# Kernel tuning notes

Measured on AMD Instinct MI355X. Metric: run time of the kernel, lower is better.

Reference implementation:

```python
import jax, jax.numpy as jnp
import numpy as np

N = 50000
E = 600000
D = 128


def setup_inputs() -> dict:
    key = jax.random.key(0)
    ks = jax.random.split(key, 10)
    scale = 1.0 / np.sqrt(D)
    inp = {
        "x": jax.random.normal(ks[0], (N, D), dtype=jnp.float32),
        "edge_index": jax.random.randint(ks[1], (2, E), 0, N, dtype=jnp.int64),
        # layer 0: fc + res_fc (residual=True, activation=relu)
        "W1": jax.random.normal(ks[2], (D, D), dtype=jnp.float32) * scale,
        "R1": jax.random.normal(ks[3], (D, D), dtype=jnp.float32) * scale,
        # layer 1
        "W2": jax.random.normal(ks[4], (D, D), dtype=jnp.float32) * scale,
        "R2": jax.random.normal(ks[5], (D, D), dtype=jnp.float32) * scale,
        # layer 2 (last, encoding=False -> no residual/activation)
        "W3": jax.random.normal(ks[6], (D, D), dtype=jnp.float32) * scale,
        # head Linear(out_dim, out_dim) with bias
        "Wh": jax.random.normal(ks[7], (D, D), dtype=jnp.float32) * scale,
        "bh": jnp.zeros((D,), dtype=jnp.float32),
    }
    return inp


def _gcn_stack(x, row, col, norm, W1, R1, W2, R2, W3, Wh, bh):
    n = x.shape[0]

    def conv(x, W, R, act):
        h = x @ W                                   # [N, D]
        msg = h[row] * norm[:, None]                # gather + per-edge scale [E+N, D]
        agg = jax.ops.segment_sum(msg, col, num_segments=n)  # scatter-add [N, D]
        if R is not None:
            agg = agg + x @ R                       # residual
        if act:
            agg = jax.nn.relu(agg)
        return agg

    x = conv(x, W1, R1, True)
    x = conv(x, W2, R2, True)
    x = conv(x, W3, None, False)
    return x @ Wh + bh


def reference(x, edge_index, W1, R1, W2, R2, W3, Wh, bh):
    n = x.shape[0]
    # add self loops (same edge structure for every layer)
    loops = jnp.arange(n, dtype=edge_index.dtype)
    row = jnp.concatenate([edge_index[0], loops])
    col = jnp.concatenate([edge_index[1], loops])
    # symmetric degree normalization: deg computed over col (incl. self loops)
    deg = jax.ops.segment_sum(jnp.ones_like(col, dtype=x.dtype), col, num_segments=n)
    dinv = deg ** -0.5
    norm = dinv[row] * dinv[col]                    # [E+N]
    return _gcn_stack(x, row, col, norm, W1, R1, W2, R2, W3, Wh, bh)
```

## Files before the change

### kernel.cpp

```cpp
#include <hip/hip_runtime.h>
#include <hip/hip_bf16.h>


#define SCAN_CHUNK 1024

typedef _Float16 half8 __attribute__((ext_vector_type(8)));
typedef _Float16 half4 __attribute__((ext_vector_type(4)));
typedef _Float16 half2v __attribute__((ext_vector_type(2)));
typedef float floatx4 __attribute__((ext_vector_type(4)));

__global__ void zero_int_kernel(int* __restrict__ p, int n) {
    int i = blockIdx.x * blockDim.x + threadIdx.x;
    if (i < n) p[i] = 0;
}

__global__ void hist_kernel(const int* __restrict__ col, int* __restrict__ cnt, int E) {
    int i = blockIdx.x * blockDim.x + threadIdx.x;
    if (i < E) atomicAdd(&cnt[col[i]], 1);
}

__global__ void dinv_kernel(const int* __restrict__ cnt, float* __restrict__ dinv, int n) {
    int i = blockIdx.x * blockDim.x + threadIdx.x;
    if (i < n) dinv[i] = rsqrtf((float)(cnt[i] + 1));
}

__global__ __launch_bounds__(256) void scan_reduce_kernel(
        const int* __restrict__ cnt, int* __restrict__ bsum, int n) {
    __shared__ int s[256];
    int b = blockIdx.x, t = threadIdx.x;
    int base = b * SCAN_CHUNK + t * 4;
    int v = 0;
    if (base + 3 < n) {
        int4 q = *(const int4*)&cnt[base];
        v = q.x + q.y + q.z + q.w;
    } else {
        for (int i = 0; i < 4; ++i) if (base + i < n) v += cnt[base + i];
    }
    s[t] = v;
    __syncthreads();
    for (int off = 128; off > 0; off >>= 1) {
        if (t < off) s[t] += s[t + off];
        __syncthreads();
    }
    if (t == 0) bsum[b] = s[0];
}

__global__ __launch_bounds__(1024) void scan_bsum_kernel(
        const int* __restrict__ bsum, int* __restrict__ boff, int nb) {
    __shared__ int s[1024];
    int t = threadIdx.x;
    s[t] = (t < nb) ? bsum[t] : 0;
    __syncthreads();
    for (int off = 1; off < 1024; off <<= 1) {
        int add = (t >= off) ? s[t - off] : 0;
        __syncthreads();
        s[t] += add;
        __syncthreads();
    }
    if (t < nb) boff[t] = (t == 0) ? 0 : s[t - 1];
}

__global__ __launch_bounds__(256) void scan_write_kernel(
        const int* __restrict__ cnt, const int* __restrict__ boff,
        int* __restrict__ row_ptr, int* __restrict__ cursor, int n, int E) {
    __shared__ int s[256];
    int b = blockIdx.x, t = threadIdx.x;
    int base = b * SCAN_CHUNK + t * 4;
    int v[4];
    int sum = 0;
    for (int i = 0; i < 4; ++i) {
        v[i] = (base + i < n) ? cnt[base + i] : 0;
        sum += v[i];
    }
    s[t] = sum;
    __syncthreads();
    for (int off = 1; off < 256; off <<= 1) {
        int add = (t >= off) ? s[t - off] : 0;
        __syncthreads();
        s[t] += add;
        __syncthreads();
    }
    int prefix = boff[b] + ((t == 0) ? 0 : s[t - 1]);
    for (int i = 0; i < 4; ++i) {
        if (base + i < n) {
            row_ptr[base + i] = prefix;
            cursor[base + i] = prefix;
            prefix += v[i];
        }
    }
    if (b == 0 && t == 0) row_ptr[n] = E;
}

__global__ void fill_kernel(const int* __restrict__ row, const int* __restrict__ colv,
                            const float* __restrict__ dinv, int* __restrict__ cursor,
                            int2* __restrict__ csr, int E) {
    int i = blockIdx.x * blockDim.x + threadIdx.x;
    if (i < E) {
        int r = row[i], c = colv[i];
        int p = atomicAdd(&cursor[c], 1);
        float nrm = dinv[r] * dinv[c];
        csr[p] = make_int2(r, __float_as_int(nrm));
    }
}

__global__ __launch_bounds__(256) void wcvt_kernel(
        const float* __restrict__ W1, const float* __restrict__ R1,
        const float* __restrict__ W2, const float* __restrict__ R2,
        const float* __restrict__ W3, const float* __restrict__ Wh,
        _Float16* __restrict__ Wt) {
    __shared__ float tile[32][33];
    int b = blockIdx.x;
    int mat = b >> 4, tl = b & 15;
    const float* W = (mat == 0) ? W1 : (mat == 1) ? R1 : (mat == 2) ? W2
                   : (mat == 3) ? R2 : (mat == 4) ? W3 : Wh;
    _Float16* T = Wt + (size_t)mat * 16384;
    int tr = (tl >> 2) * 32, tc = (tl & 3) * 32;
    int t = threadIdx.x;
    int i = t >> 3, j4 = t & 7;
    float4 v = *(const float4*)&W[(tr + i) * 128 + tc + j4 * 4];
    tile[i][j4 * 4 + 0] = v.x;
    tile[i][j4 * 4 + 1] = v.y;
    tile[i][j4 * 4 + 2] = v.z;
    tile[i][j4 * 4 + 3] = v.w;
    __syncthreads();
    half4 h;
    h.x = (_Float16)tile[j4 * 4 + 0][i];
    h.y = (_Float16)tile[j4 * 4 + 1][i];
    h.z = (_Float16)tile[j4 * 4 + 2][i];
    h.w = (_Float16)tile[j4 * 4 + 3][i];
    *(half4*)&T[(tc + i) * 128 + tr + j4 * 4] = h;
}

__global__ void cvt_kernel(const float* __restrict__ x, _Float16* __restrict__ xh, int n) {
    int i = (blockIdx.x * blockDim.x + threadIdx.x) * 4;
    if (i + 3 < n) {
        float4 v = *(const float4*)&x[i];
        half4 h;
        h.x = (_Float16)v.x; h.y = (_Float16)v.y;
        h.z = (_Float16)v.z; h.w = (_Float16)v.w;
        *(half4*)&xh[i] = h;
    } else {
        for (int j = i; j < n; ++j) xh[j] = (_Float16)x[j];
    }
}

__global__ __launch_bounds__(256) void gemm_h_kernel(
        const _Float16* __restrict__ X, const _Float16* __restrict__ Wt,
        _Float16* __restrict__ out, int n) {
    __shared__ _Float16 Af[64 * 136];
    __shared__ _Float16 Bt[128 * 136];
    int t = threadIdx.x;
    int r0 = blockIdx.x * 64;

#pragma unroll
    for (int i = 0; i < 4; ++i) {
        int flat = i * 256 + t;
        int r = flat >> 4, k8 = flat & 15;
        half8 v = {0, 0, 0, 0, 0, 0, 0, 0};
        if (r0 + r < n) v = *(const half8*)&X[(size_t)(r0 + r) * 128 + k8 * 8];
        *(half8*)&Af[r * 136 + k8 * 8] = v;
    }
#pragma unroll
    for (int i = 0; i < 8; ++i) {
        int flat = i * 256 + t;
        int c = flat >> 4, k8 = flat & 15;
        *(half8*)&Bt[c * 136 + k8 * 8] = *(const half8*)&Wt[c * 128 + k8 * 8];
    }
    __syncthreads();

    int lane = t & 63, w = t >> 6;
    int m = lane & 15, q = lane >> 4;

    floatx4 acc[8];
#pragma unroll
    for (int nt = 0; nt < 8; ++nt) acc[nt] = (floatx4){0.f, 0.f, 0.f, 0.f};

#pragma unroll
    for (int s = 0; s < 4; ++s) {
        half8 a = *(const half8*)&Af[(w * 16 + m) * 136 + s * 32 + q * 8];
#pragma unroll
        for (int nt = 0; nt < 8; ++nt) {
            half8 b = *(const half8*)&Bt[(nt * 16 + m) * 136 + s * 32 + q * 8];
            acc[nt] = __builtin_amdgcn_mfma_f32_16x16x32_f16(a, b, acc[nt], 0, 0, 0);
        }
    }

    int rowb = r0 + w * 16 + q * 4;
#pragma unroll
    for (int nt = 0; nt < 8; ++nt) {
        int col = nt * 16 + m;
#pragma unroll
        for (int r = 0; r < 4; ++r) {
            int gr = rowb + r;
            if (gr < n) out[(size_t)gr * 128 + col] = (_Float16)acc[nt][r];
        }
    }
}

__global__ __launch_bounds__(256) void gemm_f_kernel(
        const _Float16* __restrict__ X, const _Float16* __restrict__ Wt,
        const float* __restrict__ bias, float* __restrict__ out, int n) {
    __shared__ _Float16 Af[64 * 136];
    __shared__ _Float16 Bt[128 * 136];
    int t = threadIdx.x;
    int r0 = blockIdx.x * 64;

#pragma unroll
    for (int i = 0; i < 4; ++i) {
        int flat = i * 256 + t;
        int r = flat >> 4, k8 = flat & 15;
        half8 v = {0, 0, 0, 0, 0, 0, 0, 0};
        if (r0 + r < n) v = *(const half8*)&X[(size_t)(r0 + r) * 128 + k8 * 8];
        *(half8*)&Af[r * 136 + k8 * 8] = v;
    }
#pragma unroll
    for (int i = 0; i < 8; ++i) {
        int flat = i * 256 + t;
        int c = flat >> 4, k8 = flat & 15;
        *(half8*)&Bt[c * 136 + k8 * 8] = *(const half8*)&Wt[c * 128 + k8 * 8];
    }
    __syncthreads();

    int lane = t & 63, w = t >> 6;
    int m = lane & 15, q = lane >> 4;

    floatx4 acc[8];
#pragma unroll
    for (int nt = 0; nt < 8; ++nt) acc[nt] = (floatx4){0.f, 0.f, 0.f, 0.f};

#pragma unroll
    for (int s = 0; s < 4; ++s) {
        half8 a = *(const half8*)&Af[(w * 16 + m) * 136 + s * 32 + q * 8];
#pragma unroll
        for (int nt = 0; nt < 8; ++nt) {
            half8 b = *(const half8*)&Bt[(nt * 16 + m) * 136 + s * 32 + q * 8];
            acc[nt] = __builtin_amdgcn_mfma_f32_16x16x32_f16(a, b, acc[nt], 0, 0, 0);
        }
    }

    int rowb = r0 + w * 16 + q * 4;
#pragma unroll
    for (int nt = 0; nt < 8; ++nt) {
        int col = nt * 16 + m;
        float bb = bias[col];
#pragma unroll
        for (int r = 0; r < 4; ++r) {
            int gr = rowb + r;
            if (gr < n) out[(size_t)gr * 128 + col] = acc[nt][r] + bb;
        }
    }
}

__global__ void spmm_kernel(const _Float16* __restrict__ h, const _Float16* __restrict__ xr,
                            const int* __restrict__ row_ptr, const int2* __restrict__ csr,
                            const float* __restrict__ dinv, _Float16* __restrict__ out,
                            int n, int do_relu) {
    int gid = blockIdx.x * blockDim.x + threadIdx.x;
    int node = gid >> 6;
    int lane = gid & 63;
    if (node >= n) return;
    const half2v* hp = (const half2v*)h;
    float di = dinv[node];
    float w = di * di;
    half2v hv = hp[(size_t)node * 64 + lane];
    float accx = (float)hv.x * w, accy = (float)hv.y * w;
    int e = row_ptr[node], eend = row_ptr[node + 1];
    for (; e + 4 <= eend; e += 4) {
        int2 d0 = csr[e], d1 = csr[e + 1], d2 = csr[e + 2], d3 = csr[e + 3];
        half2v v0 = hp[(size_t)d0.x * 64 + lane];
        half2v v1 = hp[(size_t)d1.x * 64 + lane];
        half2v v2 = hp[(size_t)d2.x * 64 + lane];
        half2v v3 = hp[(size_t)d3.x * 64 + lane];
        float n0 = __int_as_float(d0.y), n1 = __int_as_float(d1.y);
        float n2 = __int_as_float(d2.y), n3 = __int_as_float(d3.y);
        accx = fmaf(n0, (float)v0.x, accx); accy = fmaf(n0, (float)v0.y, accy);
        accx = fmaf(n1, (float)v1.x, accx); accy = fmaf(n1, (float)v1.y, accy);
        accx = fmaf(n2, (float)v2.x, accx); accy = fmaf(n2, (float)v2.y, accy);
        accx = fmaf(n3, (float)v3.x, accx); accy = fmaf(n3, (float)v3.y, accy);
    }
    for (; e < eend; ++e) {
        int2 ed = csr[e];
        float nrm = __int_as_float(ed.y);
        half2v v = hp[(size_t)ed.x * 64 + lane];
        accx = fmaf(nrm, (float)v.x, accx);
        accy = fmaf(nrm, (float)v.y, accy);
    }
    if (xr) {
        half2v r = ((const half2v*)xr)[(size_t)node * 64 + lane];
        accx += (float)r.x;
        accy += (float)r.y;
    }
    if (do_relu) {
        accx = fmaxf(accx, 0.f);
        accy = fmaxf(accy, 0.f);
    }
    half2v o;
    o.x = (_Float16)accx;
    o.y = (_Float16)accy;
    ((half2v*)out)[(size_t)node * 64 + lane] = o;
}

extern "C" void kernel_launch(void* const* d_in, const int* in_sizes, int n_in,
                              void* d_out, int out_size, void* d_ws, size_t ws_size,
                              hipStream_t stream) {
    const float* x  = (const float*)d_in[0];
    const int*   ei = (const int*)d_in[1];
    const float* W1 = (const float*)d_in[2];
    const float* R1 = (const float*)d_in[3];
    const float* W2 = (const float*)d_in[4];
    const float* R2 = (const float*)d_in[5];
    const float* W3 = (const float*)d_in[6];
    const float* Wh = (const float*)d_in[7];
    const float* bh = (const float*)d_in[8];
    float* out = (float*)d_out;

    int N = in_sizes[0] / 128;
    int E = in_sizes[1] / 2;

    char* p = (char*)d_ws;
    auto alloc = [&](size_t bytes) {
        char* r = p;
        p += (bytes + 255) & ~(size_t)255;
        return r;
    };
    int*      cnt     = (int*)alloc((size_t)N * 4);
    int*      row_ptr = (int*)alloc((size_t)(N + 1) * 4);
    int*      cursor  = (int*)alloc((size_t)N * 4);
    float*    dinv    = (float*)alloc((size_t)N * 4);
    int*      bsum    = (int*)alloc((size_t)1024 * 4);
    int*      boff    = (int*)alloc((size_t)1024 * 4);
    int2*     csr     = (int2*)alloc((size_t)E * 8);
    _Float16* Wt      = (_Float16*)alloc((size_t)6 * 16384 * 2);
    _Float16* xh      = (_Float16*)alloc((size_t)N * 128 * 2);
    _Float16* B0h     = (_Float16*)alloc((size_t)N * 128 * 2);
    _Float16* B1h     = (_Float16*)alloc((size_t)N * 128 * 2);
    _Float16* B2h     = (_Float16*)alloc((size_t)N * 128 * 2);

    const int* rowi = ei;
    const int* coli = ei + E;

    int nb = (N + SCAN_CHUNK - 1) / SCAN_CHUNK;

    zero_int_kernel<<<(N + 255) / 256, 256, 0, stream>>>(cnt, N);
    hist_kernel<<<(E + 255) / 256, 256, 0, stream>>>(coli, cnt, E);
    dinv_kernel<<<(N + 255) / 256, 256, 0, stream>>>(cnt, dinv, N);
    scan_reduce_kernel<<<nb, 256, 0, stream>>>(cnt, bsum, N);
    scan_bsum_kernel<<<1, 1024, 0, stream>>>(bsum, boff, nb);
    scan_write_kernel<<<nb, 256, 0, stream>>>(cnt, boff, row_ptr, cursor, N, E);
    fill_kernel<<<(E + 255) / 256, 256, 0, stream>>>(rowi, coli, dinv, cursor, csr, E);
    wcvt_kernel<<<96, 256, 0, stream>>>(W1, R1, W2, R2, W3, Wh, Wt);
    cvt_kernel<<<(N * 128 / 4 + 255) / 256, 256, 0, stream>>>(x, xh, N * 128);

    int gb = (N + 63) / 64;
    int sb = (N + 3) / 4;
    _Float16* Wt1 = Wt;
    _Float16* Rt1 = Wt + 16384;
    _Float16* Wt2 = Wt + 2 * 16384;
    _Float16* Rt2 = Wt + 3 * 16384;
    _Float16* Wt3 = Wt + 4 * 16384;
    _Float16* Wth = Wt + 5 * 16384;

    gemm_h_kernel<<<gb, 256, 0, stream>>>(xh, Wt1, B0h, N);
    gemm_h_kernel<<<gb, 256, 0, stream>>>(xh, Rt1, B1h, N);
    spmm_kernel<<<sb, 256, 0, stream>>>(B0h, B1h, row_ptr, csr, dinv, B1h, N, 1);
    gemm_h_kernel<<<gb, 256, 0, stream>>>(B1h, Wt2, B0h, N);
    gemm_h_kernel<<<gb, 256, 0, stream>>>(B1h, Rt2, B2h, N);
    spmm_kernel<<<sb, 256, 0, stream>>>(B0h, B2h, row_ptr, csr, dinv, B2h, N, 1);
    gemm_h_kernel<<<gb, 256, 0, stream>>>(B2h, Wt3, B0h, N);
    spmm_kernel<<<sb, 256, 0, stream>>>(B0h, nullptr, row_ptr, csr, dinv, B1h, N, 0);
    gemm_f_kernel<<<gb, 256, 0, stream>>>(B1h, Wth, bh, out, N);
}
```

Before: 340.0 us.

## Fuse dual GEMMs with fp32 input conversion and widen SpMM edge parallelism

Merges the W and residual GEMMs of each layer into one kernel that loads the input tile once and reuses it for both weight matrices. The first layer converts the fp32 input to fp16 inside the GEMM tile load, so the separate conversion kernel and its buffer are dropped. The SpMM now splits each wavefront into four 16-lane groups that each gather a different edge with 16-byte half8 loads, then reduces the groups with cross-lane shuffles. This raises memory-level parallelism in the gather at the cost of extra shuffle work and masked tail iterations.

```diff
diff --git a/kernel.cpp b/kernel.cpp
--- a/kernel.cpp
+++ b/kernel.cpp
@@ -6,7 +6,6 @@
 
 typedef _Float16 half8 __attribute__((ext_vector_type(8)));
 typedef _Float16 half4 __attribute__((ext_vector_type(4)));
-typedef _Float16 half2v __attribute__((ext_vector_type(2)));
 typedef float floatx4 __attribute__((ext_vector_type(4)));
 
 __global__ void zero_int_kernel(int* __restrict__ p, int n) {
@@ -131,16 +130,102 @@
     *(half4*)&T[(tc + i) * 128 + tr + j4 * 4] = h;
 }
 
-__global__ void cvt_kernel(const float* __restrict__ x, _Float16* __restrict__ xh, int n) {
-    int i = (blockIdx.x * blockDim.x + threadIdx.x) * 4;
-    if (i + 3 < n) {
-        float4 v = *(const float4*)&x[i];
-        half4 h;
-        h.x = (_Float16)v.x; h.y = (_Float16)v.y;
-        h.z = (_Float16)v.z; h.w = (_Float16)v.w;
-        *(half4*)&xh[i] = h;
+template <int F32IN>
+__global__ __launch_bounds__(256) void gemm_dual_kernel(
+        const void* __restrict__ Xv, const _Float16* __restrict__ WtA,
+        const _Float16* __restrict__ WtB, _Float16* __restrict__ outA,
+        _Float16* __restrict__ outB, int n) {
+    __shared__ _Float16 Af[64 * 136];
+    __shared__ _Float16 Bt[128 * 136];
+    int t = threadIdx.x;
+    int r0 = blockIdx.x * 64;
+
+    if (F32IN) {
+        const float* X = (const float*)Xv;
+#pragma unroll
+        for (int i = 0; i < 8; ++i) {
+            int flat = i * 256 + t;
+            int r = flat >> 5, c4 = flat & 31;
+            float4 v = make_float4(0.f, 0.f, 0.f, 0.f);
+            if (r0 + r < n) v = ((const float4*)X)[(size_t)(r0 + r) * 32 + c4];
+            half4 h;
+            h.x = (_Float16)v.x; h.y = (_Float16)v.y;
+            h.z = (_Float16)v.z; h.w = (_Float16)v.w;
+            *(half4*)&Af[r * 136 + c4 * 4] = h;
+        }
     } else {
-        for (int j = i; j < n; ++j) xh[j] = (_Float16)x[j];
+        const _Float16* X = (const _Float16*)Xv;
+#pragma unroll
+        for (int i = 0; i < 4; ++i) {
+            int flat = i * 256 + t;
+            int r = flat >> 4, k8 = flat & 15;
+            half8 v = {0, 0, 0, 0, 0, 0, 0, 0};
+            if (r0 + r < n) v = *(const half8*)&X[(size_t)(r0 + r) * 128 + k8 * 8];
+            *(half8*)&Af[r * 136 + k8 * 8] = v;
+        }
+    }
+#pragma unroll
+    for (int i = 0; i < 8; ++i) {
+        int flat = i * 256 + t;
+        int c = flat >> 4, k8 = flat & 15;
+        *(half8*)&Bt[c * 136 + k8 * 8] = *(const half8*)&WtA[c * 128 + k8 * 8];
+    }
+    __syncthreads();
+
+    int lane = t & 63, w = t >> 6;
+    int m = lane & 15, q = lane >> 4;
+    int rowb = r0 + w * 16 + q * 4;
+
+    half8 a[4];
+#pragma unroll
+    for (int s = 0; s < 4; ++s)
+        a[s] = *(const half8*)&Af[(w * 16 + m) * 136 + s * 32 + q * 8];
+
+    floatx4 acc[8];
+#pragma unroll
+    for (int nt = 0; nt < 8; ++nt) acc[nt] = (floatx4){0.f, 0.f, 0.f, 0.f};
+#pragma unroll
+    for (int s = 0; s < 4; ++s)
+#pragma unroll
+        for (int nt = 0; nt < 8; ++nt) {
+            half8 b = *(const half8*)&Bt[(nt * 16 + m) * 136 + s * 32 + q * 8];
+            acc[nt] = __builtin_amdgcn_mfma_f32_16x16x32_f16(a[s], b, acc[nt], 0, 0, 0);
+        }
+    __syncthreads();
+#pragma unroll
+    for (int i = 0; i < 8; ++i) {
+        int flat = i * 256 + t;
+        int c = flat >> 4, k8 = flat & 15;
+        *(half8*)&Bt[c * 136 + k8 * 8] = *(const half8*)&WtB[c * 128 + k8 * 8];
+    }
+#pragma unroll
+    for (int nt = 0; nt < 8; ++nt) {
+        int col = nt * 16 + m;
+#pragma unroll
+        for (int r = 0; r < 4; ++r) {
+            int gr = rowb + r;
+            if (gr < n) outA[(size_t)gr * 128 + col] = (_Float16)acc[nt][r];
+        }
+    }
+    __syncthreads();
+
+#pragma unroll
+    for (int nt = 0; nt < 8; ++nt) acc[nt] = (floatx4){0.f, 0.f, 0.f, 0.f};
+#pragma unroll
+    for (int s = 0; s < 4; ++s)
+#pragma unroll
+        for (int nt = 0; nt < 8; ++nt) {
+            half8 b = *(const half8*)&Bt[(nt * 16 + m) * 136 + s * 32 + q * 8];
+            acc[nt] = __builtin_amdgcn_mfma_f32_16x16x32_f16(a[s], b, acc[nt], 0, 0, 0);
+        }
+#pragma unroll
+    for (int nt = 0; nt < 8; ++nt) {
+        int col = nt * 16 + m;
+#pragma unroll
+        for (int r = 0; r < 4; ++r) {
+            int gr = rowb + r;
+            if (gr < n) outB[(size_t)gr * 128 + col] = (_Float16)acc[nt][r];
+        }
     }
 }
 
@@ -259,45 +344,71 @@
     int node = gid >> 6;
     int lane = gid & 63;
     if (node >= n) return;
-    const half2v* hp = (const half2v*)h;
-    float di = dinv[node];
-    float w = di * di;
-    half2v hv = hp[(size_t)node * 64 + lane];
-    float accx = (float)hv.x * w, accy = (float)hv.y * w;
-    int e = row_ptr[node], eend = row_ptr[node + 1];
-    for (; e + 4 <= eend; e += 4) {
-        int2 d0 = csr[e], d1 = csr[e + 1], d2 = csr[e + 2], d3 = csr[e + 3];
-        half2v v0 = hp[(size_t)d0.x * 64 + lane];
-        half2v v1 = hp[(size_t)d1.x * 64 + lane];
-        half2v v2 = hp[(size_t)d2.x * 64 + lane];
-        half2v v3 = hp[(size_t)d3.x * 64 + lane];
+    int sub = lane >> 4;
+    int fl = lane & 15;
+    const half8* hp8 = (const half8*)h;
+
+    float acc[8];
+#pragma unroll
+    for (int j = 0; j < 8; ++j) acc[j] = 0.f;
+
+    int e0 = row_ptr[node], e1 = row_ptr[node + 1];
+    int e = e0;
+    for (; e + 16 <= e1; e += 16) {
+        int2 d0 = csr[e + sub];
+        int2 d1 = csr[e + 4 + sub];
+        int2 d2 = csr[e + 8 + sub];
+        int2 d3 = csr[e + 12 + sub];
+        half8 v0 = hp8[(size_t)d0.x * 16 + fl];
+        half8 v1 = hp8[(size_t)d1.x * 16 + fl];
+        half8 v2 = hp8[(size_t)d2.x * 16 + fl];
+        half8 v3 = hp8[(size_t)d3.x * 16 + fl];
         float n0 = __int_as_float(d0.y), n1 = __int_as_float(d1.y);
         float n2 = __int_as_float(d2.y), n3 = __int_as_float(d3.y);
-        accx = fmaf(n0, (float)v0.x, accx); accy = fmaf(n0, (float)v0.y, accy);
-        accx = fmaf(n1, (float)v1.x, accx); accy = fmaf(n1, (float)v1.y, accy);
-        accx = fmaf(n2, (float)v2.x, accx); accy = fmaf(n2, (float)v2.y, accy);
-        accx = fmaf(n3, (float)v3.x, accx); accy = fmaf(n3, (float)v3.y, accy);
-    }
-    for (; e < eend; ++e) {
-        int2 ed = csr[e];
-        float nrm = __int_as_float(ed.y);
-        half2v v = hp[(size_t)ed.x * 64 + lane];
-        accx = fmaf(nrm, (float)v.x, accx);
-        accy = fmaf(nrm, (float)v.y, accy);
-    }
-    if (xr) {
-        half2v r = ((const half2v*)xr)[(size_t)node * 64 + lane];
-        accx += (float)r.x;
-        accy += (float)r.y;
-    }
-    if (do_relu) {
-        accx = fmaxf(accx, 0.f);
-        accy = fmaxf(accy, 0.f);
-    }
-    half2v o;
-    o.x = (_Float16)accx;
-    o.y = (_Float16)accy;
-    ((half2v*)out)[(size_t)node * 64 + lane] = o;
+#pragma unroll
+        for (int j = 0; j < 8; ++j) {
+            acc[j] = fmaf(n0, (float)v0[j], acc[j]);
+            acc[j] = fmaf(n1, (float)v1[j], acc[j]);
+            acc[j] = fmaf(n2, (float)v2[j], acc[j]);
+            acc[j] = fmaf(n3, (float)v3[j], acc[j]);
+        }
+    }
+    for (; e < e1; e += 4) {
+        int idx = e + sub;
+        int act = idx < e1;
+        int cidx = act ? idx : (e1 - 1);
+        int2 d = csr[cidx];
+        float nrm = act ? __int_as_float(d.y) : 0.f;
+        half8 v = hp8[(size_t)d.x * 16 + fl];
+#pragma unroll
+        for (int j = 0; j < 8; ++j) acc[j] = fmaf(nrm, (float)v[j], acc[j]);
+    }
+#pragma unroll
+    for (int j = 0; j < 8; ++j) {
+        acc[j] += __shfl_xor(acc[j], 16, 64);
+        acc[j] += __shfl_xor(acc[j], 32, 64);
+    }
+
+    float di = dinv[node];
+    if (sub == 0) {
+        float w = di * di;
+        half8 hv = hp8[(size_t)node * 16 + fl];
+#pragma unroll
+        for (int j = 0; j < 8; ++j) acc[j] = fmaf(w, (float)hv[j], acc[j]);
+        if (xr) {
+            half8 r = ((const half8*)xr)[(size_t)node * 16 + fl];
+#pragma unroll
+            for (int j = 0; j < 8; ++j) acc[j] += (float)r[j];
+        }
+        if (do_relu) {
+#pragma unroll
+            for (int j = 0; j < 8; ++j) acc[j] = fmaxf(acc[j], 0.f);
+        }
+        half8 o;
+#pragma unroll
+        for (int j = 0; j < 8; ++j) o[j] = (_Float16)acc[j];
+        ((half8*)out)[(size_t)node * 16 + fl] = o;
+    }
 }
 
 extern "C" void kernel_launch(void* const* d_in, const int* in_sizes, int n_in,
@@ -331,7 +442,6 @@
     int*      boff    = (int*)alloc((size_t)1024 * 4);
     int2*     csr     = (int2*)alloc((size_t)E * 8);
     _Float16* Wt      = (_Float16*)alloc((size_t)6 * 16384 * 2);
-    _Float16* xh      = (_Float16*)alloc((size_t)N * 128 * 2);
     _Float16* B0h     = (_Float16*)alloc((size_t)N * 128 * 2);
     _Float16* B1h     = (_Float16*)alloc((size_t)N * 128 * 2);
     _Float16* B2h     = (_Float16*)alloc((size_t)N * 128 * 2);
@@ -349,7 +459,6 @@
     scan_write_kernel<<<nb, 256, 0, stream>>>(cnt, boff, row_ptr, cursor, N, E);
     fill_kernel<<<(E + 255) / 256, 256, 0, stream>>>(rowi, coli, dinv, cursor, csr, E);
     wcvt_kernel<<<96, 256, 0, stream>>>(W1, R1, W2, R2, W3, Wh, Wt);
-    cvt_kernel<<<(N * 128 / 4 + 255) / 256, 256, 0, stream>>>(x, xh, N * 128);
 
     int gb = (N + 63) / 64;
     int sb = (N + 3) / 4;
@@ -360,11 +469,9 @@
     _Float16* Wt3 = Wt + 4 * 16384;
     _Float16* Wth = Wt + 5 * 16384;
 
-    gemm_h_kernel<<<gb, 256, 0, stream>>>(xh, Wt1, B0h, N);
-    gemm_h_kernel<<<gb, 256, 0, stream>>>(xh, Rt1, B1h, N);
+    gemm_dual_kernel<1><<<gb, 256, 0, stream>>>(x, Wt1, Rt1, B0h, B1h, N);
     spmm_kernel<<<sb, 256, 0, stream>>>(B0h, B1h, row_ptr, csr, dinv, B1h, N, 1);
-    gemm_h_kernel<<<gb, 256, 0, stream>>>(B1h, Wt2, B0h, N);
-    gemm_h_kernel<<<gb, 256, 0, stream>>>(B1h, Rt2, B2h, N);
+    gemm_dual_kernel<0><<<gb, 256, 0, stream>>>(B1h, Wt2, Rt2, B0h, B2h, N);
     spmm_kernel<<<sb, 256, 0, stream>>>(B0h, B2h, row_ptr, csr, dinv, B2h, N, 1);
     gemm_h_kernel<<<gb, 256, 0, stream>>>(B2h, Wt3, B0h, N);
     spmm_kernel<<<sb, 256, 0, stream>>>(B0h, nullptr, row_ptr, csr, dinv, B1h, N, 0);
```

Result: faster. 317.2 us (-6.7%).
